# Optimization experiments

Hardware: AMD Instinct MI355X
Metric: run time of the kernel (lower is better)

## Reference

```python
import jax, jax.numpy as jnp
import numpy as np

LRELU = 0.01
EPS = 1e-5
HEADS = 4


def _ln(x, g, b):
    m = x.mean(-1, keepdims=True)
    v = ((x - m) ** 2).mean(-1, keepdims=True)
    return (x - m) / jnp.sqrt(v + EPS) * g + b


def _mapx(x, w1, b1, g1, be1, w2, b2, g2, be2, w3, b3):
    h = jax.nn.leaky_relu(_ln(x @ w1 + b1, g1, be1), LRELU)
    h = jax.nn.leaky_relu(_ln(h @ w2 + b2, g2, be2), LRELU)
    return h @ w3 + b3


def _mcab(x, y, wq, bq, wk, bk, wv, bv, wo, bo, rescale):
    # spectral (channel-wise) multi-head cross attention: q from x, k/v from y
    b, c, h, w = x.shape
    n = h * w
    xt = x.reshape(b, c, n).transpose(0, 2, 1)  # (b, n, c)
    yt = y.reshape(b, c, n).transpose(0, 2, 1)
    dh = c // HEADS
    q = (xt @ wq + bq).reshape(b, n, HEADS, dh).transpose(0, 2, 3, 1)  # (b,H,dh,n)
    k = (yt @ wk + bk).reshape(b, n, HEADS, dh).transpose(0, 2, 3, 1)
    v = (yt @ wv + bv).reshape(b, n, HEADS, dh).transpose(0, 2, 3, 1)
    q = q / (jnp.linalg.norm(q, axis=-1, keepdims=True) + 1e-8)
    k = k / (jnp.linalg.norm(k, axis=-1, keepdims=True) + 1e-8)
    attn = jax.nn.softmax(jnp.einsum('bhdn,bhen->bhde', q, k) * rescale, axis=-1)  # (b,H,dh,dh)
    out = jnp.einsum('bhde,bhen->bhdn', attn, v)  # (b,H,dh,n)
    out = out.transpose(0, 3, 1, 2).reshape(b, n, c) @ wo + bo
    out = out + xt  # residual
    return out.transpose(0, 2, 1).reshape(b, c, h, w)


def setup_inputs() -> dict:
    key = jax.random.key(0)
    ks = jax.random.split(key, 16)
    B, C, H, W, K = 4, 64, 128, 128, 21
    s = 0.02
    nrm = lambda k, shape: jax.random.normal(k, shape, jnp.float32) * s
    return {
        'x': jax.random.normal(ks[0], (B, C, H, W), jnp.float32),
        'semantic': jax.random.uniform(ks[1], (B, K, H, W), jnp.float32),
        'wa': nrm(ks[2], (1, C, 4)), 'ba': jnp.zeros((1, 4), jnp.float32),
        'wb': nrm(ks[3], (20, C, 3)), 'bb': jnp.zeros((20, 3), jnp.float32),
        'in_w': nrm(ks[4], (C, C)), 'in_b': jnp.zeros((C,), jnp.float32),
        'mx_w1': nrm(ks[5], (C, 2 * C)), 'mx_b1': jnp.zeros((2 * C,), jnp.float32),
        'mx_g1': jnp.ones((2 * C,), jnp.float32), 'mx_be1': jnp.zeros((2 * C,), jnp.float32),
        'mx_w2': nrm(ks[6], (2 * C, 2 * C)), 'mx_b2': jnp.zeros((2 * C,), jnp.float32),
        'mx_g2': jnp.ones((2 * C,), jnp.float32), 'mx_be2': jnp.zeros((2 * C,), jnp.float32),
        'mx_w3': nrm(ks[7], (2 * C, C)), 'mx_b3': jnp.zeros((C,), jnp.float32),
        'wq': nrm(ks[8], (C, C)), 'bq': jnp.zeros((C,), jnp.float32),
        'wk': nrm(ks[9], (C, C)), 'bk': jnp.zeros((C,), jnp.float32),
        'wv': nrm(ks[10], (C, C)), 'bv': jnp.zeros((C,), jnp.float32),
        'wo': nrm(ks[11], (C, C)), 'bo': jnp.zeros((C,), jnp.float32),
        'rescale': jnp.ones((HEADS, 1, 1), jnp.float32),
    }


def reference(x, semantic, wa, ba, wb, bb, in_w, in_b,
              mx_w1, mx_b1, mx_g1, mx_be1, mx_w2, mx_b2, mx_g2, mx_be2,
              mx_w3, mx_b3, wq, bq, wk, bk, wv, bv, wo, bo, rescale):
    sem = jax.nn.relu(semantic)            # (b,K,h,w)
    xh = x.transpose(0, 2, 3, 1)           # (b,h,w,c)
    # per-class mask-multiply: (b,K,h,w,c)
    masked = xh[:, None] * sem[:, :, :, :, None]
    # class 0 gets the extra channel (64 = 1*4 + 20*3)
    feat_a = jnp.einsum('bkhwc,kcd->bkhwd', masked[:, :1], wa) + ba[None, :, None, None, :]
    feat_b = jnp.einsum('bkhwc,kcd->bkhwd', masked[:, 1:], wb) + bb[None, :, None, None, :]
    b, _, h, w, _ = feat_a.shape
    feat_a = feat_a.reshape(b, h, w, 4)
    feat_b = jnp.moveaxis(feat_b, 1, 3).reshape(b, h, w, 60)  # preserve class order
    all_feat = jnp.concatenate([feat_a, feat_b], axis=-1)     # (b,h,w,64)
    y = (all_feat @ in_w + in_b).transpose(0, 3, 1, 2)        # (b,c,h,w)
    xm = _mapx(xh, mx_w1, mx_b1, mx_g1, mx_be1, mx_w2, mx_b2, mx_g2, mx_be2, mx_w3, mx_b3)
    xm = xm.transpose(0, 3, 1, 2)
    return _mcab(xm, y, wq, bq, wk, bk, wv, bv, wo, bo, rescale)
```

## Files before the change

kernel.cpp:

```cpp
#include <hip/hip_runtime.h>
#include <hip/hip_bf16.h>

#define NPX 16384
typedef __attribute__((ext_vector_type(8))) short short8;
typedef __attribute__((ext_vector_type(8))) _Float16 half8;
typedef __attribute__((ext_vector_type(4))) _Float16 half4;
typedef __attribute__((ext_vector_type(4))) float f32x4;

#define DEV static __device__ __forceinline__

#define WAB   0
#define WINW  4096
#define W1T   8192
#define W2T   16384
#define W3T   32768
#define WQT   40960
#define WKV   45056
#define WTOT  53248
#define NZERO 4608

DEV float lrelu(float v) { return v >= 0.f ? v : 0.01f * v; }
DEV short f2h(float f) { _Float16 h = (_Float16)f; return __builtin_bit_cast(short, h); }
DEV float h2f(short s) { return (float)__builtin_bit_cast(_Float16, s); }
DEV f32x4 mfmah(half8 a, half8 b, f32x4 c) {
    return __builtin_amdgcn_mfma_f32_16x16x32_f16(a, b, c, 0, 0, 0);
}

template<int K, int NT, int M>
DEV void gemmM(const short* __restrict__ A, int pitch,
               const short* __restrict__ WT, f32x4 (&acc)[M][NT])
{
    int lane = threadIdx.x & 63;
    int ln = lane & 15, q8 = (lane >> 4) * 8;
    const short* bp = WT + ln * K + q8;
    const short* ap = A + (size_t)ln * pitch + q8;
#pragma unroll
    for (int c0 = 0; c0 < K; c0 += 32) {
        half8 a[M];
#pragma unroll
        for (int m = 0; m < M; ++m)
            a[m] = *(const half8*)(ap + m * 16 * pitch + c0);
#pragma unroll
        for (int t = 0; t < NT; ++t) {
            half8 b = *(const half8*)(bp + (size_t)t * 16 * K + c0);
#pragma unroll
            for (int m = 0; m < M; ++m) acc[m][t] = mfmah(a[m], b, acc[m][t]);
        }
    }
}

template<int NT, int M>
DEV void acc_biasM(f32x4 (&acc)[M][NT], const float* __restrict__ bias)
{
    int ln = threadIdx.x & 15;
#pragma unroll
    for (int t = 0; t < NT; ++t) {
        float bv = bias[t * 16 + ln];
        f32x4 v = {bv, bv, bv, bv};
#pragma unroll
        for (int m = 0; m < M; ++m) acc[m][t] = v;
    }
}

template<int NT, int M>
DEV void dstoreM(const f32x4 (&acc)[M][NT], short* sD, int pitch)
{
    int lane = threadIdx.x & 63;
    int ln = lane & 15, r0 = (lane >> 4) * 4;
#pragma unroll
    for (int m = 0; m < M; ++m)
#pragma unroll
        for (int t = 0; t < NT; ++t)
#pragma unroll
            for (int r = 0; r < 4; ++r)
                sD[(m * 16 + r0 + r) * pitch + t * 16 + ln] = f2h(acc[m][t][r]);
}

template<int NT, int M>
DEV void ln_regM(f32x4 (&acc)[M][NT], const float* __restrict__ g, const float* __restrict__ be)
{
    int lane = threadIdx.x & 63, ln = lane & 15;
#pragma unroll
    for (int m = 0; m < M; ++m) {
        f32x4 s = {0,0,0,0}, ss = {0,0,0,0};
#pragma unroll
        for (int t = 0; t < NT; ++t)
#pragma unroll
            for (int r = 0; r < 4; ++r) { float v = acc[m][t][r]; s[r] += v; ss[r] += v * v; }
#pragma unroll
        for (int off = 1; off < 16; off <<= 1)
#pragma unroll
            for (int r = 0; r < 4; ++r) {
                s[r] += __shfl_xor(s[r], off);
                ss[r] += __shfl_xor(ss[r], off);
            }
        f32x4 mm, rs;
#pragma unroll
        for (int r = 0; r < 4; ++r) {
            float mean = s[r] * (1.f / 128.f);
            float var = ss[r] * (1.f / 128.f) - mean * mean;
            mm[r] = mean; rs[r] = rsqrtf(var + 1e-5f);
        }
#pragma unroll
        for (int t = 0; t < NT; ++t) {
            float gg = g[t * 16 + ln], bb = be[t * 16 + ln];
#pragma unroll
            for (int r = 0; r < 4; ++r)
                acc[m][t][r] = lrelu((acc[m][t][r] - mm[r]) * rs[r] * gg + bb);
        }
    }
}

template<int ROWS>
DEV void copyoutR(const short* sD, int pitch, short* __restrict__ dst)
{
    int lane = threadIdx.x & 63;
#pragma unroll
    for (int it = 0; it < ROWS / 8; ++it) {
        int idx = it * 512 + lane * 8;
        int px = idx >> 6, c = idx & 63;
        short8 v = *(const short8*)(&sD[px * pitch + c]);
        *reinterpret_cast<short8*>(dst + (size_t)px * 64 + c) = v;
    }
}

__global__ __launch_bounds__(256) void k_prep(const float* __restrict__ wa,
                                              const float* __restrict__ wb,
                                              const float* __restrict__ in_w,
                                              const float* __restrict__ w1,
                                              const float* __restrict__ w2,
                                              const float* __restrict__ w3,
                                              const float* __restrict__ wq,
                                              const float* __restrict__ wk,
                                              const float* __restrict__ wv,
                                              short* __restrict__ wt,
                                              float* __restrict__ gz)
{
    int idx = blockIdx.x * 256 + threadIdx.x;
    if (idx >= WTOT) {
        int z = idx - WTOT;
        if (z < NZERO) gz[z] = 0.f;
        return;
    }
    float v;
    if (idx < WINW) {
        int j = idx >> 6, c = idx & 63;
        v = (j < 4) ? wa[c * 4 + j] : wb[((j - 4) / 3) * 192 + c * 3 + ((j - 4) % 3)];
    } else if (idx < W1T) {
        int i = idx - WINW; v = in_w[(i & 63) * 64 + (i >> 6)];
    } else if (idx < W2T) {
        int i = idx - W1T; v = w1[(i & 63) * 128 + (i >> 6)];
    } else if (idx < W3T) {
        int i = idx - W2T; v = w2[(i & 127) * 128 + (i >> 7)];
    } else if (idx < WQT) {
        int i = idx - W3T; v = w3[(i & 127) * 64 + (i >> 7)];
    } else if (idx < WKV) {
        int i = idx - WQT; v = wq[(i & 63) * 64 + (i >> 6)];
    } else {
        int i = idx - WKV; int e = i >> 6, k = i & 63;
        v = (e < 64) ? wk[k * 64 + e] : wv[k * 64 + (e - 64)];
    }
    wt[idx] = f2h(v);
}

__global__ __launch_bounds__(256, 4) void k_main(const float* __restrict__ x,
                                                 const float* __restrict__ sem,
                                                 const float* __restrict__ ba,
                                                 const float* __restrict__ bbv,
                                                 const float* __restrict__ in_b,
                                                 const float* __restrict__ b1,
                                                 const float* __restrict__ g1,
                                                 const float* __restrict__ be1,
                                                 const float* __restrict__ b2,
                                                 const float* __restrict__ g2,
                                                 const float* __restrict__ be2,
                                                 const float* __restrict__ b3,
                                                 const float* __restrict__ bq,
                                                 const float* __restrict__ bk,
                                                 const float* __restrict__ bv,
                                                 const short* __restrict__ wt,
                                                 short* __restrict__ vout,
                                                 short* __restrict__ xmout,
                                                 float* __restrict__ gram,
                                                 float* __restrict__ nsq)
{
    __shared__ short blob[2][8960];
    const int tid = threadIdx.x, w = tid >> 6, lane = tid & 63;
    const int ln = lane & 15, qd = lane >> 4, r0 = qd * 4;
    const int g = w & 1, role = w >> 1;
    const int pw = blockIdx.x * 64 + g * 32;
    const int b = pw >> 14, n0 = pw & (NPX - 1);
    const float* xb = x + (size_t)b * 64 * NPX;
    short* X  = blob[g];
    short* T  = blob[g] + 2304;
    short* H  = blob[g] + 4608;
    short* KT = X;
    float* scr = (float*)T;

    {
        float vb[16];
#pragma unroll
        for (int t = 0; t < 16; ++t)
            vb[t] = xb[(size_t)(qd * 16 + t) * NPX + n0 + role * 16 + ln];
        short8 lo, hi;
#pragma unroll
        for (int t = 0; t < 8; ++t) { lo[t] = f2h(vb[t]); hi[t] = f2h(vb[8 + t]); }
        *reinterpret_cast<short8*>(&X[(role * 16 + ln) * 72 + qd * 16]) = lo;
        *reinterpret_cast<short8*>(&X[(role * 16 + ln) * 72 + qd * 16 + 8]) = hi;
    }
    __syncthreads();

    f32x4 acc8[2][8];
    if (role == 0) {
        acc_biasM<8, 2>(acc8, b1);
        gemmM<64, 8, 2>(X, 72, wt + W1T, acc8);
    } else {
        f32x4 a1f[2][4];
        {
            f32x4 z = {0,0,0,0};
#pragma unroll
            for (int m = 0; m < 2; ++m)
#pragma unroll
                for (int t = 0; t < 4; ++t) a1f[m][t] = z;
        }
        gemmM<64, 4, 2>(X, 72, wt + WAB, a1f);
#pragma unroll
        for (int t = 0; t < 4; ++t) {
            int j = t * 16 + ln;
            int cls = (j < 4) ? 0 : 1 + (j - 4) / 3;
            float bias = (j < 4) ? ba[j] : bbv[j - 4];
#pragma unroll
            for (int m = 0; m < 2; ++m) {
                f32x4 sm4 = *(const f32x4*)(sem + ((size_t)b * 21 + cls) * NPX + n0 + m * 16 + r0);
#pragma unroll
                for (int r = 0; r < 4; ++r)
                    T[(m * 16 + r0 + r) * 72 + j] = f2h(fmaxf(sm4[r], 0.f) * a1f[m][t][r] + bias);
            }
        }
    }
    __syncthreads();

    f32x4 aqreg[2][4];
    if (role == 0) {
        ln_regM<8, 2>(acc8, g1, be1);
        dstoreM<8, 2>(acc8, H, 136);
        acc_biasM<8, 2>(acc8, b2);
        gemmM<128, 8, 2>(H, 136, wt + W2T, acc8);
        ln_regM<8, 2>(acc8, g2, be2);
        dstoreM<8, 2>(acc8, H, 136);
        f32x4 a4[2][4];
        acc_biasM<4, 2>(a4, b3);
        gemmM<128, 4, 2>(H, 136, wt + W3T, a4);
        dstoreM<4, 2>(a4, H, 72);
        copyoutR<32>(H, 72, xmout + (size_t)pw * 64);
        acc_biasM<4, 2>(aqreg, bq);
        gemmM<64, 4, 2>(H, 72, wt + WQT, aqreg);
    } else {
        f32x4 a4[2][4];
        acc_biasM<4, 2>(a4, in_b);
        gemmM<64, 4, 2>(T, 72, wt + WINW, a4);
        dstoreM<4, 2>(a4, T, 72);
        f32x4 a3[2][8];
#pragma unroll
        for (int t = 0; t < 8; ++t) {
            float bvv = (t < 4) ? bk[t * 16 + ln] : bv[(t - 4) * 16 + ln];
            f32x4 vv = {bvv, bvv, bvv, bvv};
            a3[0][t] = vv; a3[1][t] = vv;
        }
        gemmM<64, 8, 2>(T, 72, wt + WKV, a3);
#pragma unroll
        for (int h = 0; h < 4; ++h) {
            f32x4 akk = {0, 0, 0, 0};
#pragma unroll
            for (int m = 0; m < 2; ++m) {
                half8 ka8 = {0, 0, 0, 0, 0, 0, 0, 0};
#pragma unroll
                for (int r = 0; r < 4; ++r) {
                    short hv = f2h(a3[m][h][r]);
                    KT[(h * 16 + ln) * 32 + m * 16 + r0 + r] = hv;
                    ka8[r] = __builtin_bit_cast(_Float16, hv);
                }
                akk = mfmah(ka8, ka8, akk);
            }
#pragma unroll
            for (int r = 0; r < 4; ++r)
                if (ln == r0 + r) scr[h * 16 + r0 + r] = akk[r];
        }
#pragma unroll
        for (int t = 4; t < 8; ++t)
#pragma unroll
            for (int m = 0; m < 2; ++m)
#pragma unroll
                for (int r = 0; r < 4; ++r)
                    vout[(size_t)(pw + m * 16 + r0 + r) * 64 + (t - 4) * 16 + ln] = f2h(a3[m][t][r]);
    }
    __syncthreads();

    if (role == 0) {
#pragma unroll
        for (int h = 0; h < 4; ++h) {
            f32x4 aqk = {0,0,0,0}, aqq = {0,0,0,0};
#pragma unroll
            for (int m = 0; m < 2; ++m) {
                half4 kv4 = *(const half4*)(&KT[(h * 16 + ln) * 32 + m * 16 + r0]);
                half8 qa8 = {0, 0, 0, 0, 0, 0, 0, 0};
                half8 ka8 = {0, 0, 0, 0, 0, 0, 0, 0};
#pragma unroll
                for (int r = 0; r < 4; ++r) {
                    qa8[r] = (_Float16)aqreg[m][h][r];
                    ka8[r] = kv4[r];
                }
                aqk = mfmah(qa8, ka8, aqk);
                aqq = mfmah(qa8, qa8, aqq);
            }
#pragma unroll
            for (int r = 0; r < 4; ++r) {
                int d = r0 + r;
                scr[64 + h * 256 + d * 16 + ln] = aqk[r];
                if (ln == d) scr[1088 + h * 16 + d] = aqq[r];
            }
        }
    }
    __syncthreads();

    const float* s0 = (const float*)(blob[0] + 2304);
    const float* s1 = (const float*)(blob[1] + 2304);
#pragma unroll
    for (int i = 0; i < 4; ++i) {
        int idx = i * 256 + tid;
        atomicAdd(&gram[(size_t)b * 1024 + idx], s0[64 + idx] + s1[64 + idx]);
    }
    if (tid < 64) {
        atomicAdd(&nsq[b * 64 + tid], s0[1088 + tid] + s1[1088 + tid]);
    } else if (tid < 128) {
        int t2 = tid - 64;
        atomicAdd(&nsq[256 + b * 64 + t2], s0[t2] + s1[t2]);
    }
}

__global__ __launch_bounds__(256) void k_attnM(const float* __restrict__ gram,
                                               const float* __restrict__ nsq,
                                               const float* __restrict__ rescale,
                                               const float* __restrict__ wo,
                                               short* __restrict__ MT)
{
    __shared__ float s_at[1024];
    int b = blockIdx.x, tid = threadIdx.x;
    if (tid < 64) {
        int h = tid >> 4, d = tid & 15;
        float nq = sqrtf(nsq[b * 64 + h * 16 + d]) + 1e-8f;
        float rsc = rescale[h];
        float lg[16];
#pragma unroll
        for (int e = 0; e < 16; ++e) {
            float nk = sqrtf(nsq[256 + b * 64 + h * 16 + e]) + 1e-8f;
            lg[e] = rsc * gram[b * 1024 + h * 256 + d * 16 + e] / (nq * nk);
        }
        float m = lg[0];
#pragma unroll
        for (int e = 1; e < 16; ++e) m = fmaxf(m, lg[e]);
        float ssum = 0.f;
#pragma unroll
        for (int e = 0; e < 16; ++e) { lg[e] = expf(lg[e] - m); ssum += lg[e]; }
        float inv = 1.f / ssum;
#pragma unroll
        for (int e = 0; e < 16; ++e) s_at[h * 256 + d * 16 + e] = lg[e] * inv;
    }
    __syncthreads();
    int he = tid >> 2, h = he >> 4, e = he & 15;
    int cc0 = (tid & 3) * 16;
#pragma unroll
    for (int cx = 0; cx < 16; ++cx) {
        int cc = cc0 + cx;
        float s = 0.f;
#pragma unroll
        for (int d = 0; d < 16; ++d)
            s = fmaf(s_at[h * 256 + d * 16 + e], wo[(h * 16 + d) * 64 + cc], s);
        MT[b * 4096 + cc * 64 + he] = f2h(s);
    }
}

__global__ __launch_bounds__(256) void k_out(const short* __restrict__ v,
                                             const short* __restrict__ xm,
                                             const short* __restrict__ MT,
                                             const float* __restrict__ bo,
                                             float* __restrict__ out)
{
    int tid = threadIdx.x, w = tid >> 6, lane = tid & 63;
    int ln = lane & 15, qd = lane >> 4;
    int pw = blockIdx.x * 64 + w * 16;
    int b = pw >> 14, n0 = pw & (NPX - 1);

    f32x4 acc[1][4];
    acc_biasM<4, 1>(acc, bo);
    gemmM<64, 4, 1>(v + (size_t)pw * 64, 64, MT + b * 4096, acc);

#pragma unroll
    for (int t = 0; t < 4; ++t) {
        int c = t * 16 + ln;
        f32x4 o;
#pragma unroll
        for (int r = 0; r < 4; ++r)
            o[r] = acc[0][t][r] + h2f(xm[(size_t)(pw + qd * 4 + r) * 64 + c]);
        *reinterpret_cast<f32x4*>(out + ((size_t)b * 64 + c) * NPX + n0 + qd * 4) = o;
    }
}

extern "C" void kernel_launch(void* const* d_in, const int* in_sizes, int n_in,
                              void* d_out, int out_size, void* d_ws, size_t ws_size,
                              hipStream_t stream)
{
    const float* x    = (const float*)d_in[0];
    const float* sem  = (const float*)d_in[1];
    const float* wa   = (const float*)d_in[2];
    const float* ba   = (const float*)d_in[3];
    const float* wb   = (const float*)d_in[4];
    const float* bbv  = (const float*)d_in[5];
    const float* in_w = (const float*)d_in[6];
    const float* in_b = (const float*)d_in[7];
    const float* w1   = (const float*)d_in[8];
    const float* b1   = (const float*)d_in[9];
    const float* g1   = (const float*)d_in[10];
    const float* be1  = (const float*)d_in[11];
    const float* w2   = (const float*)d_in[12];
    const float* b2   = (const float*)d_in[13];
    const float* g2   = (const float*)d_in[14];
    const float* be2  = (const float*)d_in[15];
    const float* w3   = (const float*)d_in[16];
    const float* b3   = (const float*)d_in[17];
    const float* wq   = (const float*)d_in[18];
    const float* bq   = (const float*)d_in[19];
    const float* wk   = (const float*)d_in[20];
    const float* bk   = (const float*)d_in[21];
    const float* wv   = (const float*)d_in[22];
    const float* bv   = (const float*)d_in[23];
    const float* wo   = (const float*)d_in[24];
    const float* bo   = (const float*)d_in[25];
    const float* rescale = (const float*)d_in[26];

    char* wsb = (char*)d_ws;
    short* wt   = (short*)wsb;
    short* vpx  = (short*)(wsb + (1u << 20));
    short* xmp  = (short*)(wsb + (1u << 20) + (8u << 20));
    float* gram = (float*)(wsb + (1u << 20) + (16u << 20));
    float* nsq  = gram + 4096;
    short* MT   = (short*)(nsq + 512);

    dim3 blk(256);
    k_prep<<<dim3(226), blk, 0, stream>>>(wa, wb, in_w, w1, w2, w3, wq, wk, wv, wt, gram);
    k_main<<<dim3(1024), blk, 0, stream>>>(x, sem, ba, bbv, in_b,
                                           b1, g1, be1, b2, g2, be2, b3, bq, bk, bv,
                                           wt, vpx, xmp, gram, nsq);
    k_attnM<<<dim3(4), blk, 0, stream>>>(gram, nsq, rescale, wo, MT);
    k_out<<<dim3(1024), blk, 0, stream>>>(vpx, xmp, MT, bo, (float*)d_out);
}
```

Before: 178.9 us.

## Store weights and intermediates in MFMA fragment order for coalesced loads

Weights are now pre-permuted in k_prep into per-lane MFMA fragment order, so each B-operand load in gemmM is one contiguous 16-byte read per lane instead of a strided gather. The v and xm intermediates are also written in fragment-tiled layouts, and MT is stored the same way. This lets k_out read its operands as contiguous vectors in place of scattered 2-byte element loads and removes the LDS copy-out pass. The cost is more complex index maths in the producer kernels, plus scattered LDS writes when staging v.

Measured after the change: 162.9 us (median of 2 runs). 9.0% less time.

```diff
diff --git a/kernel.cpp b/kernel.cpp
--- a/kernel.cpp
+++ b/kernel.cpp
@@ -28,12 +28,12 @@
 
 template<int K, int NT, int M>
 DEV void gemmM(const short* __restrict__ A, int pitch,
-               const short* __restrict__ WT, f32x4 (&acc)[M][NT])
+               const short* __restrict__ WB, f32x4 (&acc)[M][NT])
 {
     int lane = threadIdx.x & 63;
     int ln = lane & 15, q8 = (lane >> 4) * 8;
-    const short* bp = WT + ln * K + q8;
     const short* ap = A + (size_t)ln * pitch + q8;
+    const short* bp = WB + lane * 8;
 #pragma unroll
     for (int c0 = 0; c0 < K; c0 += 32) {
         half8 a[M];
@@ -42,7 +42,7 @@
             a[m] = *(const half8*)(ap + m * 16 * pitch + c0);
 #pragma unroll
         for (int t = 0; t < NT; ++t) {
-            half8 b = *(const half8*)(bp + (size_t)t * 16 * K + c0);
+            half8 b = *(const half8*)(bp + (((c0 >> 5) * NT + t) << 9));
 #pragma unroll
             for (int m = 0; m < M; ++m) acc[m][t] = mfmah(a[m], b, acc[m][t]);
         }
@@ -108,19 +108,6 @@
             for (int r = 0; r < 4; ++r)
                 acc[m][t][r] = lrelu((acc[m][t][r] - mm[r]) * rs[r] * gg + bb);
         }
-    }
-}
-
-template<int ROWS>
-DEV void copyoutR(const short* sD, int pitch, short* __restrict__ dst)
-{
-    int lane = threadIdx.x & 63;
-#pragma unroll
-    for (int it = 0; it < ROWS / 8; ++it) {
-        int idx = it * 512 + lane * 8;
-        int px = idx >> 6, c = idx & 63;
-        short8 v = *(const short8*)(&sD[px * pitch + c]);
-        *reinterpret_cast<short8*>(dst + (size_t)px * 64 + c) = v;
     }
 }
 
@@ -142,22 +129,35 @@
         if (z < NZERO) gz[z] = 0.f;
         return;
     }
+    int base, ETl;
+    if      (idx < WINW) { base = WAB;  ETl = 4; }
+    else if (idx < W1T)  { base = WINW; ETl = 4; }
+    else if (idx < W2T)  { base = W1T;  ETl = 8; }
+    else if (idx < W3T)  { base = W2T;  ETl = 8; }
+    else if (idx < WQT)  { base = W3T;  ETl = 4; }
+    else if (idx < WKV)  { base = WQT;  ETl = 4; }
+    else                 { base = WKV;  ETl = 8; }
+    int i = idx - base;
+    int frag = i >> 9, wi = i & 511;
+    int lane = wi >> 3, kk = wi & 7;
+    int ln = lane & 15, qd = lane >> 4;
+    int cs = frag / ETl, t = frag % ETl;
+    int e = t * 16 + ln;
+    int k = cs * 32 + qd * 8 + kk;
     float v;
-    if (idx < WINW) {
-        int j = idx >> 6, c = idx & 63;
-        v = (j < 4) ? wa[c * 4 + j] : wb[((j - 4) / 3) * 192 + c * 3 + ((j - 4) % 3)];
-    } else if (idx < W1T) {
-        int i = idx - WINW; v = in_w[(i & 63) * 64 + (i >> 6)];
-    } else if (idx < W2T) {
-        int i = idx - W1T; v = w1[(i & 63) * 128 + (i >> 6)];
-    } else if (idx < W3T) {
-        int i = idx - W2T; v = w2[(i & 127) * 128 + (i >> 7)];
-    } else if (idx < WQT) {
-        int i = idx - W3T; v = w3[(i & 127) * 64 + (i >> 7)];
-    } else if (idx < WKV) {
-        int i = idx - WQT; v = wq[(i & 63) * 64 + (i >> 6)];
+    if (base == WAB) {
+        v = (e < 4) ? wa[k * 4 + e] : wb[((e - 4) / 3) * 192 + k * 3 + ((e - 4) % 3)];
+    } else if (base == WINW) {
+        v = in_w[k * 64 + e];
+    } else if (base == W1T) {
+        v = w1[k * 128 + e];
+    } else if (base == W2T) {
+        v = w2[k * 128 + e];
+    } else if (base == W3T) {
+        v = w3[k * 64 + e];
+    } else if (base == WQT) {
+        v = wq[k * 64 + e];
     } else {
-        int i = idx - WKV; int e = i >> 6, k = i & 63;
         v = (e < 64) ? wk[k * 64 + e] : wv[k * 64 + (e - 64)];
     }
     wt[idx] = f2h(v);
@@ -179,8 +179,8 @@
                                                  const float* __restrict__ bk,
                                                  const float* __restrict__ bv,
                                                  const short* __restrict__ wt,
-                                                 short* __restrict__ vout,
-                                                 short* __restrict__ xmout,
+                                                 short* __restrict__ vfrag,
+                                                 short* __restrict__ xmfrag,
                                                  float* __restrict__ gram,
                                                  float* __restrict__ nsq)
 {
@@ -251,8 +251,19 @@
         f32x4 a4[2][4];
         acc_biasM<4, 2>(a4, b3);
         gemmM<128, 4, 2>(H, 136, wt + W3T, a4);
+#pragma unroll
+        for (int m = 0; m < 2; ++m) {
+            short8 lo, hi;
+#pragma unroll
+            for (int i = 0; i < 8; ++i) {
+                lo[i] = f2h(a4[m][i >> 2][i & 3]);
+                hi[i] = f2h(a4[m][2 + (i >> 2)][i & 3]);
+            }
+            size_t xbase = ((size_t)(pw >> 4) + m) * 1024 + lane * 16;
+            *reinterpret_cast<short8*>(xmfrag + xbase) = lo;
+            *reinterpret_cast<short8*>(xmfrag + xbase + 8) = hi;
+        }
         dstoreM<4, 2>(a4, H, 72);
-        copyoutR<32>(H, 72, xmout + (size_t)pw * 64);
         acc_biasM<4, 2>(aqreg, bq);
         gemmM<64, 4, 2>(H, 72, wt + WQT, aqreg);
     } else {
@@ -269,30 +280,40 @@
         }
         gemmM<64, 8, 2>(T, 72, wt + WKV, a3);
 #pragma unroll
+        for (int t = 0; t < 4; ++t)
+#pragma unroll
+            for (int m = 0; m < 2; ++m)
+#pragma unroll
+                for (int r = 0; r < 4; ++r)
+                    KT[(t * 16 + ln) * 32 + m * 16 + r0 + r] = f2h(a3[m][t][r]);
+#pragma unroll
+        for (int t = 4; t < 8; ++t)
+#pragma unroll
+            for (int m = 0; m < 2; ++m)
+#pragma unroll
+                for (int r = 0; r < 4; ++r)
+                    T[m * 1024 + ((t - 4) >> 1) * 512 +
+                      ((((t - 4) & 1) * 2 + (ln >> 3)) & 3) * 128 +
+                      (r0 + r) * 8 + (ln & 7)] = f2h(a3[m][t][r]);
+#pragma unroll
+        for (int it = 0; it < 4; ++it) {
+            short8 vv = *(const short8*)(&T[it * 512 + lane * 8]);
+            *reinterpret_cast<short8*>(vfrag + ((size_t)(pw >> 4)) * 1024 + it * 512 + lane * 8) = vv;
+        }
+#pragma unroll
         for (int h = 0; h < 4; ++h) {
             f32x4 akk = {0, 0, 0, 0};
 #pragma unroll
             for (int m = 0; m < 2; ++m) {
                 half8 ka8 = {0, 0, 0, 0, 0, 0, 0, 0};
 #pragma unroll
-                for (int r = 0; r < 4; ++r) {
-                    short hv = f2h(a3[m][h][r]);
-                    KT[(h * 16 + ln) * 32 + m * 16 + r0 + r] = hv;
-                    ka8[r] = __builtin_bit_cast(_Float16, hv);
-                }
+                for (int r = 0; r < 4; ++r) ka8[r] = (_Float16)a3[m][h][r];
                 akk = mfmah(ka8, ka8, akk);
             }
 #pragma unroll
             for (int r = 0; r < 4; ++r)
                 if (ln == r0 + r) scr[h * 16 + r0 + r] = akk[r];
         }
-#pragma unroll
-        for (int t = 4; t < 8; ++t)
-#pragma unroll
-            for (int m = 0; m < 2; ++m)
-#pragma unroll
-                for (int r = 0; r < 4; ++r)
-                    vout[(size_t)(pw + m * 16 + r0 + r) * 64 + (t - 4) * 16 + ln] = f2h(a3[m][t][r]);
     }
     __syncthreads();
 
@@ -369,6 +390,7 @@
     __syncthreads();
     int he = tid >> 2, h = he >> 4, e = he & 15;
     int cc0 = (tid & 3) * 16;
+    int mbase = b * 4096 + (he >> 5) * 2048 + ((he >> 3) & 3) * 128 + (he & 7);
 #pragma unroll
     for (int cx = 0; cx < 16; ++cx) {
         int cc = cc0 + cx;
@@ -376,12 +398,12 @@
 #pragma unroll
         for (int d = 0; d < 16; ++d)
             s = fmaf(s_at[h * 256 + d * 16 + e], wo[(h * 16 + d) * 64 + cc], s);
-        MT[b * 4096 + cc * 64 + he] = f2h(s);
-    }
-}
-
-__global__ __launch_bounds__(256) void k_out(const short* __restrict__ v,
-                                             const short* __restrict__ xm,
+        MT[mbase + (cc >> 4) * 512 + (cc & 15) * 8] = f2h(s);
+    }
+}
+
+__global__ __launch_bounds__(256) void k_out(const short* __restrict__ vfrag,
+                                             const short* __restrict__ xmfrag,
                                              const short* __restrict__ MT,
                                              const float* __restrict__ bo,
                                              float* __restrict__ out)
@@ -390,18 +412,39 @@
     int ln = lane & 15, qd = lane >> 4;
     int pw = blockIdx.x * 64 + w * 16;
     int b = pw >> 14, n0 = pw & (NPX - 1);
-
-    f32x4 acc[1][4];
-    acc_biasM<4, 1>(acc, bo);
-    gemmM<64, 4, 1>(v + (size_t)pw * 64, 64, MT + b * 4096, acc);
-
+    size_t tile = (size_t)(pw >> 4);
+
+    f32x4 acc[4];
+    {
+#pragma unroll
+        for (int t = 0; t < 4; ++t) {
+            float bv = bo[t * 16 + ln];
+            f32x4 v = {bv, bv, bv, bv};
+            acc[t] = v;
+        }
+    }
+    const short* ap = vfrag + tile * 1024 + lane * 8;
+    const short* bp = MT + b * 4096 + lane * 8;
+#pragma unroll
+    for (int cs = 0; cs < 2; ++cs) {
+        half8 a = *(const half8*)(ap + cs * 512);
+#pragma unroll
+        for (int t = 0; t < 4; ++t) {
+            half8 bfr = *(const half8*)(bp + ((cs * 4 + t) << 9));
+            acc[t] = mfmah(a, bfr, acc[t]);
+        }
+    }
+    short8 x0 = *(const short8*)(xmfrag + tile * 1024 + lane * 16);
+    short8 x1 = *(const short8*)(xmfrag + tile * 1024 + lane * 16 + 8);
 #pragma unroll
     for (int t = 0; t < 4; ++t) {
         int c = t * 16 + ln;
         f32x4 o;
 #pragma unroll
-        for (int r = 0; r < 4; ++r)
-            o[r] = acc[0][t][r] + h2f(xm[(size_t)(pw + qd * 4 + r) * 64 + c]);
+        for (int r = 0; r < 4; ++r) {
+            short xv = (t < 2) ? x0[t * 4 + r] : x1[(t - 2) * 4 + r];
+            o[r] = acc[t][r] + h2f(xv);
+        }
         *reinterpret_cast<f32x4*>(out + ((size_t)b * 64 + c) * NPX + n0 + qd * 4) = o;
     }
 }
```
